# Optimization experiments

Measured on AMD Instinct MI355X. Metric: run time of the kernel, lower is better.

The kernel has to match this reference:

```python
import jax, jax.numpy as jnp
import numpy as np

NDIR = 6  # build_tree.num_directions()

def prelu(x, alpha):
    return jnp.where(x >= 0, x, alpha * x)

def setup_inputs() -> dict:
    key = jax.random.key(0)
    ks = jax.random.split(key, 8)
    B, N_IN, N_OUT, IDIM, ODIM, V = 16, 16384, 8192, 128, 128, 64
    last = jax.random.normal(ks[0], (B, N_IN, IDIM), dtype=jnp.float32)
    vec = jax.random.randint(ks[1], (B, N_OUT), 0, V)
    dmap = jax.random.randint(ks[2], (V,), 0, NDIR)
    drev = jax.random.randint(ks[3], (V,), 0, 2)
    child_l = jax.random.randint(ks[4], (N_OUT,), 0, N_IN)
    child_r = jax.random.randint(ks[5], (N_OUT,), 0, N_IN)
    # stacked per-direction Linear(idim*2, odim) weights/biases
    W = jax.random.normal(ks[6], (NDIR, 2 * IDIM, ODIM), dtype=jnp.float32) * (1.0 / np.sqrt(2 * IDIM))
    b = jax.random.normal(ks[7], (NDIR, ODIM), dtype=jnp.float32) * 0.01
    alpha = jnp.array(0.005, dtype=jnp.float32)  # PReLU init weight
    return {"last": last, "W": W, "b": b, "alpha": alpha, "vec": vec,
            "dmap": dmap, "drev": drev, "child_l": child_l, "child_r": child_r}

def reference(last, W, b, alpha, vec, dmap, drev, child_l, child_r):
    # gather per-edge direction-reverse flag: [B, N_OUT, 1]
    r = drev[vec].astype(last.dtype)[:, :, None]
    lch = last[:, child_l]  # [B, N_OUT, IDIM]
    rch = last[:, child_r]  # [B, N_OUT, IDIM]
    # direction-masked child swap, concat -> [B, N_OUT, 2*IDIM]
    pair = jnp.concatenate([lch * (1 - r) + rch * r,
                            rch * (1 - r) + lch * r], axis=-1)
    dirs = dmap[vec][:, :, None]  # direction id per node, [B, N_OUT, 1]
    ndir = W.shape[0]
    tmp = jnp.zeros(pair.shape[:2] + (W.shape[-1],), dtype=last.dtype)
    # masked grouped GEMM: each node routed to its direction's Linear
    for i in range(ndir):  # small fixed set of relation types
        y = pair @ W[i] + b[i]
        tmp = tmp + jnp.where(dirs == i, y, jnp.zeros((), dtype=last.dtype))
    return prelu(tmp, alpha)
```

## Files before the change

### kernel.cpp

```cpp
#include <hip/hip_runtime.h>

#define NDIR  6
#define B_    16
#define N_IN  16384
#define N_OUT 8192
#define IDIM  128
#define ODIM  128
#define TOTAL (B_ * N_OUT)
#define BM    128

#define WS_CNT 0
#define WS_OFF 8
#define WS_CUR 16
#define WS_IDS 64
#define WS_WT  131584

using s16x8 = __attribute__((ext_vector_type(8))) short;
using f32x4 = __attribute__((ext_vector_type(4))) float;

__global__ void zero_kernel(int* ws) {
    int t = threadIdx.x;
    if (t < 32) ws[t] = 0;
}

__global__ void count_kernel(const int* __restrict__ vec, const int* __restrict__ dmap,
                             int* __restrict__ ws) {
    __shared__ int h[NDIR];
    int t = threadIdx.x;
    if (t < NDIR) h[t] = 0;
    __syncthreads();
    int id = blockIdx.x * 256 + t;
    if (id < TOTAL) {
        int d = dmap[vec[id]];
        atomicAdd(&h[d], 1);
    }
    __syncthreads();
    if (t < NDIR && h[t]) atomicAdd(&ws[WS_CNT + t], h[t]);
}

__global__ void prefix_kernel(int* ws) {
    if (threadIdx.x == 0) {
        int acc = 0;
        for (int i = 0; i < NDIR; ++i) {
            ws[WS_OFF + i] = acc;
            ws[WS_CUR + i] = acc;
            acc += ws[WS_CNT + i];
        }
        ws[WS_OFF + NDIR] = acc;
    }
}

__global__ void scatter_kernel(const int* __restrict__ vec, const int* __restrict__ dmap,
                               int* __restrict__ ws) {
    __shared__ int h[NDIR];
    __shared__ int base[NDIR];
    int t = threadIdx.x;
    if (t < NDIR) h[t] = 0;
    __syncthreads();
    int id = blockIdx.x * 256 + t;
    int d = 0, pos = 0;
    if (id < TOTAL) {
        d = dmap[vec[id]];
        pos = atomicAdd(&h[d], 1);
    }
    __syncthreads();
    if (t < NDIR) base[t] = h[t] ? atomicAdd(&ws[WS_CUR + t], h[t]) : 0;
    __syncthreads();
    if (id < TOTAL) ws[WS_IDS + base[d] + pos] = id;
}

__global__ void wconvert_kernel(const float* __restrict__ W, int* __restrict__ ws) {
    unsigned short* wt = (unsigned short*)(ws + WS_WT);
    int g = blockIdx.x * 256 + threadIdx.x;
    int dsb = g >> 12;
    int e = g & 4095;
    int col = e >> 5;
    int kk = e & 31;
    int cp = kk >> 3, i = kk & 7;
    int key = (col >> 1) & 3;
    int d = dsb >> 3, s = dsb & 7;
    int ksrc = s * 32 + ((cp ^ key) << 3) + i;
    float w = W[((d * 256) + ksrc) * 128 + col];
    unsigned u = __float_as_uint(w);
    float hf = __uint_as_float(u & 0xFFFF0000u);
    float lf = w - hf;
    int base = dsb * 8192 + col * 32 + cp * 8 + i;
    wt[base] = (unsigned short)(u >> 16);
    wt[base + 4096] = (unsigned short)(__float_as_uint(lf) >> 16);
}

__device__ __forceinline__ void cvt8(float4 a, float4 b, s16x8& h, s16x8& lo) {
    float x[8] = {a.x, a.y, a.z, a.w, b.x, b.y, b.z, b.w};
    #pragma unroll
    for (int j = 0; j < 8; ++j) {
        unsigned u = __float_as_uint(x[j]);
        float hf = __uint_as_float(u & 0xFFFF0000u);
        float lf = x[j] - hf;
        h[j] = (short)(u >> 16);
        lo[j] = (short)(__float_as_uint(lf) >> 16);
    }
}

__global__ __launch_bounds__(256, 3) void gemm_kernel(
    const float* __restrict__ last, const float* __restrict__ bias,
    const float* __restrict__ alphap,
    const int* __restrict__ vec, const int* __restrict__ drev,
    const int* __restrict__ child_l, const int* __restrict__ child_r,
    const int* __restrict__ ws, float* __restrict__ out)
{
    int dir = blockIdx.y;
    int start = ws[WS_OFF + dir];
    int end   = ws[WS_OFF + dir + 1];
    int m0 = start + (int)blockIdx.x * BM;
    if (m0 >= end) return;
    const int* ids = ws + WS_IDS;

    __shared__ unsigned short wbuf[2][8192];
    __shared__ int s_row0[BM], s_row1[BM], s_oid[BM];

    int t = threadIdx.x;
    int l = t & 63;
    int wid = t >> 6;

    if (t < BM) {
        int idx = m0 + t;
        bool valid = idx < end;
        int id = ids[valid ? idx : end - 1];
        int b = id >> 13;
        int n = id & (N_OUT - 1);
        int v = vec[id];
        int r = drev[v];
        int cl = child_l[n];
        int cr = child_r[n];
        int first  = r ? cr : cl;
        int second = r ? cl : cr;
        s_row0[t] = b * N_IN + first;
        s_row1[t] = b * N_IN + second;
        s_oid[t]  = valid ? id : -1;
    }

    const char* wt_blk = (const char*)(ws + WS_WT) + (size_t)dir * 8 * 16384;

    #define STAGE_W(buf, s_)                                                     \
        {                                                                        \
            const char* gsrc = wt_blk + (size_t)(s_) * 16384 + wid * 4096 + l * 16; \
            char* ldst = (char*)&wbuf[buf][0] + wid * 4096;                      \
            _Pragma("unroll")                                                    \
            for (int i_ = 0; i_ < 4; ++i_) {                                     \
                __builtin_amdgcn_global_load_lds(                                \
                    (const __attribute__((address_space(1))) void*)(gsrc + i_ * 1024), \
                    (__attribute__((address_space(3))) void*)(ldst + i_ * 1024), \
                    16, 0, 0);                                                   \
            }                                                                    \
        }

    STAGE_W(0, 0);
    __syncthreads();

    int rowA[2][2];
    #pragma unroll
    for (int f = 0; f < 2; ++f) {
        int m = wid * 32 + f * 16 + (l & 15);
        rowA[0][f] = s_row0[m];
        rowA[1][f] = s_row1[m];
    }

    f32x4 acc[2][8];
    #pragma unroll
    for (int f = 0; f < 2; ++f)
        #pragma unroll
        for (int nf = 0; nf < 8; ++nf)
            acc[f][nf] = (f32x4){0.f, 0.f, 0.f, 0.f};

    float4 xa0[2], xa1[2];
    #pragma unroll
    for (int f = 0; f < 2; ++f) {
        const float* src = last + (size_t)rowA[0][f] * IDIM + (l >> 4) * 8;
        xa0[f] = *(const float4*)src;
        xa1[f] = *(const float4*)(src + 4);
    }

    #pragma unroll
    for (int s = 0; s < 8; ++s) {
        int cur = s & 1;
        s16x8 ah[2], al[2];
        #pragma unroll
        for (int f = 0; f < 2; ++f) cvt8(xa0[f], xa1[f], ah[f], al[f]);
        if (s < 7) {
            #pragma unroll
            for (int f = 0; f < 2; ++f) {
                const float* src = last + (size_t)rowA[(s + 1) >> 2][f] * IDIM
                                 + ((s + 1) & 3) * 32 + (l >> 4) * 8;
                xa0[f] = *(const float4*)src;
                xa1[f] = *(const float4*)(src + 4);
            }
        }
        if (s < 7) STAGE_W(cur ^ 1, s + 1);
        #pragma unroll
        for (int q = 0; q < 4; ++q) {
            s16x8 bh[2], bl[2];
            #pragma unroll
            for (int i = 0; i < 2; ++i) {
                int nf = q * 2 + i;
                int col = nf * 16 + (l & 15);
                int cp = (l >> 4) ^ ((col >> 1) & 3);
                int off = col * 32 + cp * 8;
                bh[i] = *(const s16x8*)&wbuf[cur][off];
                bl[i] = *(const s16x8*)&wbuf[cur][off + 4096];
            }
            #pragma unroll
            for (int f = 0; f < 2; ++f) {
                #pragma unroll
                for (int i = 0; i < 2; ++i) {
                    int nf = q * 2 + i;
                    acc[f][nf] = __builtin_amdgcn_mfma_f32_16x16x32_bf16(ah[f], bh[i], acc[f][nf], 0, 0, 0);
                    acc[f][nf] = __builtin_amdgcn_mfma_f32_16x16x32_bf16(ah[f], bl[i], acc[f][nf], 0, 0, 0);
                    acc[f][nf] = __builtin_amdgcn_mfma_f32_16x16x32_bf16(al[f], bh[i], acc[f][nf], 0, 0, 0);
                }
            }
        }
        __syncthreads();
    }

    float alpha = alphap[0];
    #pragma unroll
    for (int nf = 0; nf < 8; ++nf) {
        int col = nf * 16 + (l & 15);
        float bv = bias[dir * ODIM + col];
        #pragma unroll
        for (int f = 0; f < 2; ++f) {
            #pragma unroll
            for (int j = 0; j < 4; ++j) {
                int mloc = wid * 32 + f * 16 + (l >> 4) * 4 + j;
                int id = s_oid[mloc];
                if (id < 0) continue;
                float y = acc[f][nf][j] + bv;
                out[(size_t)id * ODIM + col] = y >= 0.f ? y : alpha * y;
            }
        }
    }
    #undef STAGE_W
}

extern "C" void kernel_launch(void* const* d_in, const int* in_sizes, int n_in,
                              void* d_out, int out_size, void* d_ws, size_t ws_size,
                              hipStream_t stream) {
    const float* last    = (const float*)d_in[0];
    const float* W       = (const float*)d_in[1];
    const float* bias    = (const float*)d_in[2];
    const float* alpha   = (const float*)d_in[3];
    const int*   vec     = (const int*)d_in[4];
    const int*   dmap    = (const int*)d_in[5];
    const int*   drev    = (const int*)d_in[6];
    const int*   child_l = (const int*)d_in[7];
    const int*   child_r = (const int*)d_in[8];
    float* out = (float*)d_out;
    int*   ws  = (int*)d_ws;

    zero_kernel<<<1, 64, 0, stream>>>(ws);
    count_kernel<<<TOTAL / 256, 256, 0, stream>>>(vec, dmap, ws);
    prefix_kernel<<<1, 64, 0, stream>>>(ws);
    scatter_kernel<<<TOTAL / 256, 256, 0, stream>>>(vec, dmap, ws);
    wconvert_kernel<<<(NDIR * 8 * 4096) / 256, 256, 0, stream>>>(W, ws);
    dim3 grid(TOTAL / BM, NDIR);
    gemm_kernel<<<grid, 256, 0, stream>>>(last, bias, alpha, vec, drev,
                                          child_l, child_r, ws, out);
}
```

Baseline: 85.29 us.

## Compact GEMM grid to real tiles and deepen A/W prefetch with manual waitcnt

The grid used to be TOTAL/BM x NDIR, with most blocks exiting early. It is now a 1D grid sized to the real tile count: prefix_kernel computes per-direction block offsets and each block finds its direction with a small search. The GEMM main loop gains a two-stage register double buffer for the gathered A rows, and the per-step __syncthreads is replaced by explicit s_waitcnt vmcnt plus s_barrier, so global loads stay in flight across iterations. The hand-tuned vmcnt count depends on the exact number of outstanding loads the compiler emits, and the extra A buffers add register pressure.

```diff
diff --git a/kernel.cpp b/kernel.cpp
--- a/kernel.cpp
+++ b/kernel.cpp
@@ -8,10 +8,12 @@
 #define ODIM  128
 #define TOTAL (B_ * N_OUT)
 #define BM    128
+#define MAXBLK (TOTAL / BM + NDIR)
 
 #define WS_CNT 0
 #define WS_OFF 8
 #define WS_CUR 16
+#define WS_BLK 24
 #define WS_IDS 64
 #define WS_WT  131584
 
@@ -40,13 +42,17 @@
 
 __global__ void prefix_kernel(int* ws) {
     if (threadIdx.x == 0) {
-        int acc = 0;
+        int acc = 0, bacc = 0;
         for (int i = 0; i < NDIR; ++i) {
             ws[WS_OFF + i] = acc;
             ws[WS_CUR + i] = acc;
-            acc += ws[WS_CNT + i];
+            ws[WS_BLK + i] = bacc;
+            int c = ws[WS_CNT + i];
+            acc += c;
+            bacc += (c + BM - 1) / BM;
         }
         ws[WS_OFF + NDIR] = acc;
+        ws[WS_BLK + NDIR] = bacc;
     }
 }
 
@@ -101,6 +107,8 @@
     }
 }
 
+#define CFENCE() asm volatile("" ::: "memory")
+
 __global__ __launch_bounds__(256, 3) void gemm_kernel(
     const float* __restrict__ last, const float* __restrict__ bias,
     const float* __restrict__ alphap,
@@ -108,11 +116,16 @@
     const int* __restrict__ child_l, const int* __restrict__ child_r,
     const int* __restrict__ ws, float* __restrict__ out)
 {
-    int dir = blockIdx.y;
+    int i = blockIdx.x;
+    if (i >= ws[WS_BLK + NDIR]) return;
+    int dir = 0;
+    #pragma unroll
+    for (int d = 1; d < NDIR; ++d)
+        if (i >= ws[WS_BLK + d]) dir = d;
+    int tile = i - ws[WS_BLK + dir];
     int start = ws[WS_OFF + dir];
     int end   = ws[WS_OFF + dir + 1];
-    int m0 = start + (int)blockIdx.x * BM;
-    if (m0 >= end) return;
+    int m0 = start + tile * BM;
     const int* ids = ws + WS_IDS;
 
     __shared__ unsigned short wbuf[2][8192];
@@ -138,6 +151,15 @@
         s_row1[t] = b * N_IN + second;
         s_oid[t]  = valid ? id : -1;
     }
+    __syncthreads();
+
+    int rowA[2][2];
+    #pragma unroll
+    for (int f = 0; f < 2; ++f) {
+        int m = wid * 32 + f * 16 + (l & 15);
+        rowA[0][f] = s_row0[m];
+        rowA[1][f] = s_row1[m];
+    }
 
     const char* wt_blk = (const char*)(ws + WS_WT) + (size_t)dir * 8 * 16384;
 
@@ -154,16 +176,16 @@
             }                                                                    \
         }
 
-    STAGE_W(0, 0);
-    __syncthreads();
-
-    int rowA[2][2];
-    #pragma unroll
-    for (int f = 0; f < 2; ++f) {
-        int m = wid * 32 + f * 16 + (l & 15);
-        rowA[0][f] = s_row0[m];
-        rowA[1][f] = s_row1[m];
-    }
+    #define ISSUE_A(buf, s_)                                                     \
+        {                                                                        \
+            _Pragma("unroll")                                                    \
+            for (int f_ = 0; f_ < 2; ++f_) {                                     \
+                const float* src = last + (size_t)rowA[(s_) >> 2][f_] * IDIM     \
+                                 + ((s_) & 3) * 32 + (l >> 4) * 8;               \
+                xa0[buf][f_] = *(const float4*)src;                              \
+                xa1[buf][f_] = *(const float4*)(src + 4);                        \
+            }                                                                    \
+        }
 
     f32x4 acc[2][8];
     #pragma unroll
@@ -172,54 +194,54 @@
         for (int nf = 0; nf < 8; ++nf)
             acc[f][nf] = (f32x4){0.f, 0.f, 0.f, 0.f};
 
-    float4 xa0[2], xa1[2];
-    #pragma unroll
-    for (int f = 0; f < 2; ++f) {
-        const float* src = last + (size_t)rowA[0][f] * IDIM + (l >> 4) * 8;
-        xa0[f] = *(const float4*)src;
-        xa1[f] = *(const float4*)(src + 4);
-    }
+    float4 xa0[2][2], xa1[2][2];
+
+    STAGE_W(0, 0);
+    CFENCE();
+    ISSUE_A(0, 0);
+    ISSUE_A(1, 1);
+    CFENCE();
 
     #pragma unroll
     for (int s = 0; s < 8; ++s) {
         int cur = s & 1;
+        if (s < 7) { STAGE_W(cur ^ 1, s + 1); CFENCE(); }
+        if (s < 7) { asm volatile("s_waitcnt vmcnt(8)" ::: "memory"); }
+        else       { asm volatile("s_waitcnt vmcnt(0)" ::: "memory"); }
+        __builtin_amdgcn_s_barrier();
+        CFENCE();
         s16x8 ah[2], al[2];
         #pragma unroll
-        for (int f = 0; f < 2; ++f) cvt8(xa0[f], xa1[f], ah[f], al[f]);
-        if (s < 7) {
-            #pragma unroll
-            for (int f = 0; f < 2; ++f) {
-                const float* src = last + (size_t)rowA[(s + 1) >> 2][f] * IDIM
-                                 + ((s + 1) & 3) * 32 + (l >> 4) * 8;
-                xa0[f] = *(const float4*)src;
-                xa1[f] = *(const float4*)(src + 4);
-            }
-        }
-        if (s < 7) STAGE_W(cur ^ 1, s + 1);
+        for (int f = 0; f < 2; ++f) cvt8(xa0[cur][f], xa1[cur][f], ah[f], al[f]);
+        if (s < 6) { CFENCE(); ISSUE_A(cur, s + 2); CFENCE(); }
         #pragma unroll
         for (int q = 0; q < 4; ++q) {
             s16x8 bh[2], bl[2];
             #pragma unroll
-            for (int i = 0; i < 2; ++i) {
-                int nf = q * 2 + i;
+            for (int i2 = 0; i2 < 2; ++i2) {
+                int nf = q * 2 + i2;
                 int col = nf * 16 + (l & 15);
                 int cp = (l >> 4) ^ ((col >> 1) & 3);
                 int off = col * 32 + cp * 8;
-                bh[i] = *(const s16x8*)&wbuf[cur][off];
-                bl[i] = *(const s16x8*)&wbuf[cur][off + 4096];
+                bh[i2] = *(const s16x8*)&wbuf[cur][off];
+                bl[i2] = *(const s16x8*)&wbuf[cur][off + 4096];
             }
             #pragma unroll
             for (int f = 0; f < 2; ++f) {
                 #pragma unroll
-                for (int i = 0; i < 2; ++i) {
-                    int nf = q * 2 + i;
-                    acc[f][nf] = __builtin_amdgcn_mfma_f32_16x16x32_bf16(ah[f], bh[i], acc[f][nf], 0, 0, 0);
-                    acc[f][nf] = __builtin_amdgcn_mfma_f32_16x16x32_bf16(ah[f], bl[i], acc[f][nf], 0, 0, 0);
-                    acc[f][nf] = __builtin_amdgcn_mfma_f32_16x16x32_bf16(al[f], bh[i], acc[f][nf], 0, 0, 0);
+                for (int i2 = 0; i2 < 2; ++i2) {
+                    int nf = q * 2 + i2;
+                    acc[f][nf] = __builtin_amdgcn_mfma_f32_16x16x32_bf16(ah[f], bh[i2], acc[f][nf], 0, 0, 0);
+                    acc[f][nf] = __builtin_amdgcn_mfma_f32_16x16x32_bf16(ah[f], bl[i2], acc[f][nf], 0, 0, 0);
+                    acc[f][nf] = __builtin_amdgcn_mfma_f32_16x16x32_bf16(al[f], bh[i2], acc[f][nf], 0, 0, 0);
                 }
             }
         }
-        __syncthreads();
+        if (s < 7) {
+            CFENCE();
+            __builtin_amdgcn_s_barrier();
+            CFENCE();
+        }
     }
 
     float alpha = alphap[0];
@@ -240,6 +262,7 @@
         }
     }
     #undef STAGE_W
+    #undef ISSUE_A
 }
 
 extern "C" void kernel_launch(void* const* d_in, const int* in_sizes, int n_in,
@@ -262,7 +285,6 @@
     prefix_kernel<<<1, 64, 0, stream>>>(ws);
     scatter_kernel<<<TOTAL / 256, 256, 0, stream>>>(vec, dmap, ws);
     wconvert_kernel<<<(NDIR * 8 * 4096) / 256, 256, 0, stream>>>(W, ws);
-    dim3 grid(TOTAL / BM, NDIR);
-    gemm_kernel<<<grid, 256, 0, stream>>>(last, bias, alpha, vec, drev,
-                                          child_l, child_r, ws, out);
-}
+    gemm_kernel<<<MAXBLK, 256, 0, stream>>>(last, bias, alpha, vec, drev,
+                                            child_l, child_r, ws, out);
+}
```

New measurement: 81.95 us (median of 2 runs). 1.04x faster.
